# Optimization experiments

Hardware: AMD Instinct MI355X
Metric: run time of the kernel (lower is better)

## Reference

```python
import jax, jax.numpy as jnp
import numpy as np
import math

B, S, H, NH, NKV, HD = 1, 2048, 4096, 32, 8, 128
ROPE_THETA = 10000.0


def setup_inputs() -> dict:
    key = jax.random.key(0)
    ks = jax.random.split(key, 16)
    hidden_states = jax.random.normal(ks[0], (B, S, H), jnp.float32) * 0.02
    Wq = jax.random.normal(ks[1], (NH * HD, H), jnp.float32) * 0.02
    Wk = jax.random.normal(ks[2], (NKV * HD, H), jnp.float32) * 0.02
    Wv = jax.random.normal(ks[3], (NKV * HD, H), jnp.float32) * 0.02
    Wo = jax.random.normal(ks[4], (H, NH * HD), jnp.float32) * 0.02
    # RoPE cos/sin, HF Llama convention: emb = concat(freqs, freqs)
    inv_freq = 1.0 / (ROPE_THETA ** (jnp.arange(0, HD, 2, dtype=jnp.float32) / HD))
    pos = jnp.arange(S, dtype=jnp.float32)
    freqs = pos[:, None] * inv_freq[None, :]              # [S, HD/2]
    emb = jnp.concatenate([freqs, freqs], axis=-1)        # [S, HD]
    cos = jnp.cos(emb)[None]                              # [1, S, HD]
    sin = jnp.sin(emb)[None]
    # additive causal mask [B, 1, S, S]
    causal = jnp.tril(jnp.ones((S, S), dtype=bool))
    attention_mask = jnp.where(causal, 0.0, -1e9).astype(jnp.float32)[None, None]
    # reorder permutations (as written by GPTQ act-order reordering)
    perm = lambda k, n: jax.random.permutation(k, n).astype(jnp.int32)
    return {
        'hidden_states': hidden_states, 'Wq': Wq, 'Wk': Wk, 'Wv': Wv, 'Wo': Wo,
        'cos': cos, 'sin': sin, 'attention_mask': attention_mask,
        'q_order_col': perm(ks[5], H), 'q_order_row': perm(ks[6], NH * HD),
        'k_order_col': perm(ks[7], H), 'k_order_row': perm(ks[8], NKV * HD),
        'v_order_col': perm(ks[9], H), 'v_order_row': perm(ks[10], NKV * HD),
        'o_order_col': perm(ks[11], NH * HD), 'o_order_row': perm(ks[12], H),
    }


def _rotate_half(x):
    x1, x2 = jnp.split(x, 2, axis=-1)
    return jnp.concatenate([-x2, x1], axis=-1)


def reference(hidden_states, Wq, Wk, Wv, Wo, cos, sin, attention_mask,
              q_order_col, q_order_row, k_order_col, k_order_row,
              v_order_col, v_order_row, o_order_col, o_order_row):
    bsz, q_len, _ = hidden_states.shape
    # permuted projections: gather cols of input, GEMM, gather rows of output
    q = hidden_states[:, :, q_order_col] @ Wq.T
    q = q[:, :, q_order_row]
    k = hidden_states[:, :, k_order_col] @ Wk.T
    k = k[:, :, k_order_row]
    v = hidden_states[:, :, v_order_col] @ Wv.T
    v = v[:, :, v_order_row]
    q = q.reshape(bsz, q_len, NH, HD).transpose(0, 2, 1, 3)   # [B,NH,S,HD]
    k = k.reshape(bsz, q_len, NKV, HD).transpose(0, 2, 1, 3)  # [B,NKV,S,HD]
    v = v.reshape(bsz, q_len, NKV, HD).transpose(0, 2, 1, 3)
    # RoPE
    c = cos[:, None, :, :]  # [1,1,S,HD]
    s = sin[:, None, :, :]
    q = q * c + _rotate_half(q) * s
    k = k * c + _rotate_half(k) * s
    # repeat_kv for GQA
    rep = NH // NKV
    k = jnp.repeat(k, rep, axis=1)  # [B,NH,S,HD]
    v = jnp.repeat(v, rep, axis=1)
    # eager attention: full score matrix, fp32 softmax
    scores = jnp.einsum('bhqd,bhkd->bhqk', q, k) / math.sqrt(HD)
    scores = scores + attention_mask
    probs = jax.nn.softmax(scores.astype(jnp.float32), axis=-1).astype(q.dtype)
    # dropout p=0.0 (eval) -> identity
    attn = jnp.einsum('bhqk,bhkd->bhqd', probs, v)
    attn = attn.transpose(0, 2, 1, 3).reshape(bsz, q_len, NH * HD)
    out = attn[:, :, o_order_col] @ Wo.T
    out = out[:, :, o_order_row]
    return out
```

## Files before the change

kernel.cpp:

```cpp
#include <hip/hip_runtime.h>

typedef unsigned short u16;
typedef unsigned char u8;
typedef __bf16 bf16x8 __attribute__((ext_vector_type(8)));
typedef float f32x4 __attribute__((ext_vector_type(4)));
typedef int i32x4 __attribute__((ext_vector_type(4)));
typedef int i32x8 __attribute__((ext_vector_type(8)));

__device__ __forceinline__ u16 f2bf(float f) {
    unsigned u = __float_as_uint(f);
    unsigned r = (u + 0x7fffu + ((u >> 16) & 1u)) >> 16;
    return (u16)r;
}
__device__ __forceinline__ float bf2f(u16 h) {
    return __uint_as_float(((unsigned)h) << 16);
}
__device__ __forceinline__ unsigned pack_bf2(float lo, float hi) {
    unsigned a = __float_as_uint(hi) + 0x8000u;
    unsigned b = __float_as_uint(lo) + 0x8000u;
    return __builtin_amdgcn_perm(a, b, 0x07060302u);
}
__device__ __forceinline__ unsigned pack_fp8x4(float a, float b, float c, float d) {
    unsigned w = __builtin_amdgcn_cvt_pk_fp8_f32(a, b, 0, false);
    w = __builtin_amdgcn_cvt_pk_fp8_f32(c, d, w, true);
    return w;
}
__device__ __forceinline__ void async_copy16(const void* g, void* l) {
    __builtin_amdgcn_global_load_lds((__attribute__((address_space(1))) void*)(void*)g,
                                     (__attribute__((address_space(3))) void*)l, 16, 0, 0);
}

#define FP8_SCALE 64.0f
#define FP8_UNSCALE (1.0f / 4096.0f)


__global__ void inv4_k(const int* __restrict__ q, const int* __restrict__ k,
                       const int* __restrict__ v, const int* __restrict__ o,
                       int* __restrict__ invq, int* __restrict__ invk,
                       int* __restrict__ invv, int* __restrict__ invo) {
    int i = blockIdx.x * 256 + threadIdx.x;
    int a = i >> 12, j = i & 4095;
    const int* p = a == 0 ? q : a == 1 ? k : a == 2 ? v : o;
    int* inv = a == 0 ? invq : a == 1 ? invk : a == 2 ? invv : invo;
    inv[p[j]] = j;
}

__global__ __launch_bounds__(256) void permw4_k(
    const float* __restrict__ Wq, const float* __restrict__ Wk,
    const float* __restrict__ Wv, const float* __restrict__ Wo,
    const int* __restrict__ qor, const int* __restrict__ kor,
    const int* __restrict__ vor, const int* __restrict__ oor,
    const int* __restrict__ invq, const int* __restrict__ invk,
    const int* __restrict__ invv, const int* __restrict__ invo,
    u8* __restrict__ Wqkf8, u16* __restrict__ Wvp, u16* __restrict__ Wop) {
    __shared__ float rowbuf[4096];
    int j = blockIdx.x;
    const float* W; const int* rp; const int* inv; int row; int f8;
    u8* out8 = nullptr; u16* out16 = nullptr;
    if (j < 4096)      { W = Wq; rp = qor; inv = invq; row = j;        out8 = Wqkf8 + (size_t)j * 4096; f8 = 1; }
    else if (j < 5120) { W = Wk; rp = kor; inv = invk; row = j - 4096; out8 = Wqkf8 + (size_t)j * 4096; f8 = 1; }
    else if (j < 6144) { W = Wv; rp = vor; inv = invv; row = j - 5120; out16 = Wvp + (size_t)(j - 5120) * 4096; f8 = 0; }
    else               { W = Wo; rp = oor; inv = invo; row = j - 6144; out16 = Wop + (size_t)(j - 6144) * 4096; f8 = 0; }
    if (f8) {
        int hd = row & 127, b = hd >> 4;
        row = (row & ~127) | ((hd & 15) | ((b & 1) << 6) | ((b & 2) << 3) | ((hd & 64) >> 1));
    }
    const float4* wr4 = (const float4*)(W + (size_t)rp[row] * 4096);
#pragma unroll
    for (int t = 0; t < 4; t++)
        ((float4*)rowbuf)[threadIdx.x + t * 256] = wr4[threadIdx.x + t * 256];
    __syncthreads();
    if (f8) {
        int t = threadIdx.x;
        const int4* inv4p = (const int4*)inv;
        float v[16];
#pragma unroll
        for (int u = 0; u < 4; u++) {
            int4 ix = inv4p[t * 4 + u];
            v[4 * u + 0] = rowbuf[ix.x] * FP8_SCALE;
            v[4 * u + 1] = rowbuf[ix.y] * FP8_SCALE;
            v[4 * u + 2] = rowbuf[ix.z] * FP8_SCALE;
            v[4 * u + 3] = rowbuf[ix.w] * FP8_SCALE;
        }
        uint4 wv;
        wv.x = pack_fp8x4(v[0], v[1], v[2], v[3]);
        wv.y = pack_fp8x4(v[4], v[5], v[6], v[7]);
        wv.z = pack_fp8x4(v[8], v[9], v[10], v[11]);
        wv.w = pack_fp8x4(v[12], v[13], v[14], v[15]);
        int tb = (t & ~7) | ((t & 7) ^ (j & 7));
        ((uint4*)out8)[tb] = wv;
    } else {
        unsigned* o32 = (unsigned*)out16;
        const int2* inv2 = (const int2*)inv;
#pragma unroll
        for (int t = 0; t < 8; t++) {
            int c = threadIdx.x + t * 256;
            int2 ij = inv2[c];
            o32[c] = pack_bf2(rowbuf[ij.x], rowbuf[ij.y]);
        }
    }
}

__global__ __launch_bounds__(256) void cvt_k(const float* __restrict__ x,
                                             u16* __restrict__ Xb,
                                             u8* __restrict__ Xf8) {
    int row = blockIdx.x;
    int t = threadIdx.x;
    const float4* src = (const float4*)(x + (size_t)row * 4096);
    float v[16];
#pragma unroll
    for (int u = 0; u < 4; u++) {
        float4 a = src[t * 4 + u];
        v[4 * u + 0] = a.x; v[4 * u + 1] = a.y; v[4 * u + 2] = a.z; v[4 * u + 3] = a.w;
    }
    uint4 b0, b1;
    b0.x = pack_bf2(v[0], v[1]);  b0.y = pack_bf2(v[2], v[3]);
    b0.z = pack_bf2(v[4], v[5]);  b0.w = pack_bf2(v[6], v[7]);
    b1.x = pack_bf2(v[8], v[9]);  b1.y = pack_bf2(v[10], v[11]);
    b1.z = pack_bf2(v[12], v[13]); b1.w = pack_bf2(v[14], v[15]);
    uint4* ob = (uint4*)(Xb + (size_t)row * 4096);
    ob[t * 2] = b0;
    ob[t * 2 + 1] = b1;
    uint4 w8;
    w8.x = pack_fp8x4(v[0] * FP8_SCALE, v[1] * FP8_SCALE, v[2] * FP8_SCALE, v[3] * FP8_SCALE);
    w8.y = pack_fp8x4(v[4] * FP8_SCALE, v[5] * FP8_SCALE, v[6] * FP8_SCALE, v[7] * FP8_SCALE);
    w8.z = pack_fp8x4(v[8] * FP8_SCALE, v[9] * FP8_SCALE, v[10] * FP8_SCALE, v[11] * FP8_SCALE);
    w8.w = pack_fp8x4(v[12] * FP8_SCALE, v[13] * FP8_SCALE, v[14] * FP8_SCALE, v[15] * FP8_SCALE);
    int tb = (t & ~7) | ((t & 7) ^ (row & 7));
    ((uint4*)(Xf8 + (size_t)row * 4096))[tb] = w8;
}

__global__ __launch_bounds__(256) void vtr_k(const float* __restrict__ Vpart,
                                             u16* __restrict__ Vt) {
    __shared__ u16 t[64][65];
    int bx = blockIdx.x;
    int s0 = (bx & 31) * 64, c0 = (bx >> 5) * 64;
    int x = threadIdx.x & 63, y4 = threadIdx.x >> 6;
    const float* Vp0 = Vpart;
    const float* Vp1 = Vpart + (size_t)2048 * 1024;
    for (int i = 0; i < 16; i++) {
        int r = y4 * 16 + i;
        size_t idx = (size_t)(s0 + r) * 1024 + c0 + x;
        t[r][x] = f2bf(Vp0[idx] + Vp1[idx]);
    }
    __syncthreads();
    for (int i = 0; i < 16; i++) {
        int r = y4 * 16 + i;
        int xk = 4 * (x & 15) + (x >> 4);
        Vt[(size_t)(c0 + r) * 2048 + s0 + xk] = t[x][r];
    }
}


#define QKV_BAR() asm volatile("s_barrier" ::: "memory")

#define QK_STAGE(bufi, kt) do {                                                   \
    u8* la_ = S8 + (bufi) * 32768 + w * 4096;                                     \
    u8* lb_ = la_ + 16384;                                                        \
    const int k0_ = (kt) * 128;                                                   \
    _Pragma("unroll")                                                             \
    for (int t_ = 0; t_ < 4; t_++)                                                \
        async_copy16(AgQ + (size_t)t_ * 8 * 4096 + k0_, la_ + t_ * 1024);         \
    _Pragma("unroll")                                                             \
    for (int t_ = 0; t_ < 4; t_++)                                                \
        async_copy16(BgQ + (size_t)t_ * 8 * 4096 + k0_, lb_ + t_ * 1024);         \
} while (0)

#define QK_COMPUTE(bufi) do {                                                     \
    const u8* la_ = S8 + (bufi) * 32768;                                          \
    const u8* lb_ = la_ + 16384;                                                  \
    union { i32x8 v8; i32x4 v4[2]; } u_;                                          \
    i32x8 bfv[4], af0, af1;                                                       \
    _Pragma("unroll")                                                             \
    for (int j_ = 0; j_ < 4; j_++) {                                              \
        const int r_ = (wn + j_ * 16 + l16) * 128;                                \
        u_.v4[0] = *(const i32x4*)&lb_[r_ + s0b];                                 \
        u_.v4[1] = *(const i32x4*)&lb_[r_ + s1b];                                 \
        bfv[j_] = u_.v8;                                                          \
    }                                                                             \
    { const int r_ = (wm + l16) * 128;                                            \
      u_.v4[0] = *(const i32x4*)&la_[r_ + s0b];                                   \
      u_.v4[1] = *(const i32x4*)&la_[r_ + s1b]; af0 = u_.v8; }                    \
    { const int r_ = (wm + 16 + l16) * 128;                                       \
      u_.v4[0] = *(const i32x4*)&la_[r_ + s0b];                                   \
      u_.v4[1] = *(const i32x4*)&la_[r_ + s1b]; af1 = u_.v8; }                    \
    asm volatile("s_waitcnt lgkmcnt(0)" ::: "memory");                            \
    __builtin_amdgcn_sched_barrier(0);                                            \
    __builtin_amdgcn_s_setprio(1);                                                \
    _Pragma("unroll")                                                             \
    for (int j_ = 0; j_ < 4; j_++) {                                              \
        acc[0][j_] = __builtin_amdgcn_mfma_scale_f32_16x16x128_f8f6f4(af0, bfv[j_], acc[0][j_], 0, 0, 0, 0x7F7F7F7F, 0, 0x7F7F7F7F); \
        acc[1][j_] = __builtin_amdgcn_mfma_scale_f32_16x16x128_f8f6f4(af1, bfv[j_], acc[1][j_], 0, 0, 0, 0x7F7F7F7F, 0, 0x7F7F7F7F); \
    }                                                                             \
    __builtin_amdgcn_s_setprio(0);                                                \
    { const int r_ = (wm + 32 + l16) * 128;                                       \
      u_.v4[0] = *(const i32x4*)&la_[r_ + s0b];                                   \
      u_.v4[1] = *(const i32x4*)&la_[r_ + s1b]; af0 = u_.v8; }                    \
    { const int r_ = (wm + 48 + l16) * 128;                                       \
      u_.v4[0] = *(const i32x4*)&la_[r_ + s0b];                                   \
      u_.v4[1] = *(const i32x4*)&la_[r_ + s1b]; af1 = u_.v8; }                    \
    asm volatile("s_waitcnt lgkmcnt(0)" ::: "memory");                            \
    __builtin_amdgcn_sched_barrier(0);                                            \
    __builtin_amdgcn_s_setprio(1);                                                \
    _Pragma("unroll")                                                             \
    for (int j_ = 0; j_ < 4; j_++) {                                              \
        acc[2][j_] = __builtin_amdgcn_mfma_scale_f32_16x16x128_f8f6f4(af0, bfv[j_], acc[2][j_], 0, 0, 0, 0x7F7F7F7F, 0, 0x7F7F7F7F); \
        acc[3][j_] = __builtin_amdgcn_mfma_scale_f32_16x16x128_f8f6f4(af1, bfv[j_], acc[3][j_], 0, 0, 0, 0x7F7F7F7F, 0, 0x7F7F7F7F); \
    }                                                                             \
    __builtin_amdgcn_s_setprio(0);                                                \
} while (0)

#define V_STAGE(bufi, kt) do {                                                    \
    u16* a0_ = (u16*)(S8 + (bufi) * 32768);                                       \
    u16* a1_ = a0_ + 4096;                                                        \
    u16* b0_ = a0_ + 8192;                                                        \
    u16* b1_ = a0_ + 12288;                                                       \
    const int k0_ = (kt) * 64;                                                    \
    async_copy16(AgV + k0_,                          a0_ + w * 512);              \
    async_copy16(AgV + (size_t)64 * 4096 + k0_,      a0_ + (w + 4) * 512);        \
    async_copy16(AgV + k0_ + 32,                     a1_ + w * 512);              \
    async_copy16(AgV + (size_t)64 * 4096 + k0_ + 32, a1_ + (w + 4) * 512);        \
    async_copy16(BgV + k0_,                          b0_ + w * 512);              \
    async_copy16(BgV + (size_t)64 * 4096 + k0_,      b0_ + (w + 4) * 512);        \
    async_copy16(BgV + k0_ + 32,                     b1_ + w * 512);              \
    async_copy16(BgV + (size_t)64 * 4096 + k0_ + 32, b1_ + (w + 4) * 512);        \
} while (0)

#define V_COMPUTE(bufi) do {                                                      \
    const u16* base_ = (const u16*)(S8 + (bufi) * 32768);                         \
    _Pragma("unroll")                                                             \
    for (int kk_ = 0; kk_ < 2; kk_++) {                                           \
        const u16* la_ = base_ + kk_ * 4096;                                      \
        const u16* lb_ = base_ + 8192 + kk_ * 4096;                               \
        bf16x8 af[4], bfv[4];                                                     \
        _Pragma("unroll")                                                         \
        for (int i_ = 0; i_ < 4; i_++)                                            \
            af[i_] = *(const bf16x8*)&la_[(wm + i_ * 16 + l16) * 32 + quad * 8];  \
        _Pragma("unroll")                                                         \
        for (int j_ = 0; j_ < 4; j_++)                                            \
            bfv[j_] = *(const bf16x8*)&lb_[(wn + j_ * 16 + l16) * 32 + quad * 8]; \
        asm volatile("s_waitcnt lgkmcnt(0)" ::: "memory");                        \
        __builtin_amdgcn_sched_barrier(0);                                        \
        __builtin_amdgcn_s_setprio(1);                                            \
        _Pragma("unroll")                                                         \
        for (int i_ = 0; i_ < 4; i_++)                                            \
            _Pragma("unroll")                                                     \
            for (int j_ = 0; j_ < 4; j_++)                                        \
                acc[i_][j_] = __builtin_amdgcn_mfma_f32_16x16x32_bf16(af[i_], bfv[j_], acc[i_][j_], 0, 0, 0); \
        __builtin_amdgcn_s_setprio(0);                                            \
    }                                                                             \
} while (0)

__global__ __launch_bounds__(256, 2) void gemm_qkv_k(const u8* __restrict__ Xf8,
                                                     const u16* __restrict__ Xb,
                                                     const u8* __restrict__ Wqk,
                                                     const u16* __restrict__ Wv,
                                                     u16* __restrict__ QKV,
                                                     float* __restrict__ Vpart,
                                                     const float* __restrict__ cosv,
                                                     const float* __restrict__ sinv) {
    extern __shared__ u8 S8[];
    const int tid = threadIdx.x;
    const int w = tid >> 6, lane = tid & 63;
    const int quad = lane >> 4, l16 = lane & 15;
    const int bm0 = blockIdx.y * 128;
    const int wm = (w >> 1) * 64, wn = (w & 1) * 64;
    const int swz = l16 & 7;
    const int s0b = ((quad * 2) ^ swz) * 16;
    const int s1b = ((quad * 2 + 1) ^ swz) * 16;

    if (blockIdx.x < 40) {
        const int bn0 = blockIdx.x * 128;
        const u8* AgQ = Xf8 + (size_t)(bm0 + w * 32 + (lane >> 3)) * 4096 + (lane & 7) * 16;
        const u8* BgQ = Wqk + (size_t)(bn0 + w * 32 + (lane >> 3)) * 4096 + (lane & 7) * 16;
        f32x4 acc[4][4] = {};

        QK_STAGE(0, 0);
        QK_STAGE(1, 1);
        asm volatile("s_waitcnt vmcnt(8)" ::: "memory");
        QKV_BAR();
        int cur = 0;
        for (int t = 0; t < 30; ++t) {
            QK_COMPUTE(cur);
            QKV_BAR();
            QK_STAGE(cur, t + 2);
            asm volatile("s_waitcnt vmcnt(8)" ::: "memory");
            QKV_BAR();
            cur ^= 1;
        }
        QK_COMPUTE(0);
        asm volatile("s_waitcnt vmcnt(0)" ::: "memory");
        QKV_BAR();
        QK_COMPUTE(1);

        const float qsc = (bn0 < 4096) ? 0.08838834764831845f : 1.0f;
        const int hb = (wn ? 32 : 0) + l16;
#pragma unroll
        for (int i = 0; i < 4; i++) {
            const int row = bm0 + wm + i * 16 + quad * 4;
#pragma unroll
            for (int jp = 0; jp < 2; jp++) {
                const int d1 = hb + jp * 16;
                const int ce = bn0 + wn + jp * 32 + l16;
#pragma unroll
                for (int r = 0; r < 4; r++) {
                    const int s = row + r;
                    const float c  = cosv[s * 128 + d1];
                    const float sn = sinv[s * 128 + d1];
                    const float x1 = acc[i][jp * 2][r]     * FP8_UNSCALE;
                    const float x2 = acc[i][jp * 2 + 1][r] * FP8_UNSCALE;
                    QKV[(size_t)s * 6144 + ce]      = f2bf((x1 * c - x2 * sn) * qsc);
                    QKV[(size_t)s * 6144 + ce + 16] = f2bf((x2 * c + x1 * sn) * qsc);
                }
            }
        }
    } else {
        const int vx = blockIdx.x - 40;
        const int bn0 = (vx & 7) * 128;
        const int kslice = vx >> 3;
        const int kb = kslice * 2048;
        const int r0 = w * 16 + (lane >> 2);
        const int c0 = (lane & 3) * 8;
        const u16* AgV = Xb + (size_t)(bm0 + r0) * 4096 + kb + c0;
        const u16* BgV = Wv + (size_t)(bn0 + r0) * 4096 + kb + c0;
        f32x4 acc[4][4] = {};

        V_STAGE(0, 0);
        V_STAGE(1, 1);
        asm volatile("s_waitcnt vmcnt(8)" ::: "memory");
        QKV_BAR();
        int cur = 0;
        for (int t = 0; t < 30; ++t) {
            V_COMPUTE(cur);
            QKV_BAR();
            V_STAGE(cur, t + 2);
            asm volatile("s_waitcnt vmcnt(8)" ::: "memory");
            QKV_BAR();
            cur ^= 1;
        }
        V_COMPUTE(0);
        asm volatile("s_waitcnt vmcnt(0)" ::: "memory");
        QKV_BAR();
        V_COMPUTE(1);

        float* Vp = Vpart + (size_t)kslice * 2048 * 1024;
#pragma unroll
        for (int i = 0; i < 4; i++) {
            const int row = bm0 + wm + i * 16 + quad * 4;
#pragma unroll
            for (int j = 0; j < 4; j++) {
                const int col = bn0 + wn + j * 16 + l16;
#pragma unroll
                for (int r = 0; r < 4; r++)
                    Vp[(size_t)(row + r) * 1024 + col] = acc[i][j][r];
            }
        }
    }
}


#define GO_STAGE(bufi, kt) do {                                                   \
    u16* la_ = S + (bufi) * 24576;                                                \
    u16* lb_ = la_ + 16384;                                                       \
    const int k0_ = (kt) * 64;                                                    \
    _Pragma("unroll")                                                             \
    for (int u = 0; u < 4; u++)                                                   \
        async_copy16(Asrc + (size_t)u * 64 * 4096 + k0_, la_ + u * 4096 + sdst);  \
    _Pragma("unroll")                                                             \
    for (int u = 0; u < 2; u++)                                                   \
        async_copy16(Bsrc + (size_t)u * 64 * 4096 + k0_, lb_ + u * 4096 + sdst);  \
} while (0)

#define GO_COMPUTE(bufi) do {                                                     \
    const u16* la_ = S + (bufi) * 24576;                                          \
    const u16* lb_ = la_ + 16384;                                                 \
    bf16x8 bfr[4][2], afr[2][2];                                                  \
    _Pragma("unroll")                                                             \
    for (int j = 0; j < 4; j++) {                                                 \
        const int rb_ = (wn + j * 16 + l16) * 64;                                 \
        bfr[j][0] = *(const bf16x8*)&lb_[rb_ + o0];                               \
        bfr[j][1] = *(const bf16x8*)&lb_[rb_ + o1];                               \
    }                                                                             \
    _Pragma("unroll")                                                             \
    for (int i = 0; i < 2; i++) {                                                 \
        const int ra_ = (wm + i * 16 + l16) * 64;                                 \
        afr[i][0] = *(const bf16x8*)&la_[ra_ + o0];                               \
        afr[i][1] = *(const bf16x8*)&la_[ra_ + o1];                               \
    }                                                                             \
    asm volatile("s_waitcnt lgkmcnt(0)" ::: "memory");                            \
    __builtin_amdgcn_sched_barrier(0);                                            \
    __builtin_amdgcn_s_setprio(1);                                                \
    _Pragma("unroll")                                                             \
    for (int i = 0; i < 2; i++)                                                   \
        _Pragma("unroll")                                                         \
        for (int j = 0; j < 4; j++) {                                             \
            acc[i][j] = __builtin_amdgcn_mfma_f32_16x16x32_bf16(afr[i][0], bfr[j][0], acc[i][j], 0, 0, 0); \
            acc[i][j] = __builtin_amdgcn_mfma_f32_16x16x32_bf16(afr[i][1], bfr[j][1], acc[i][j], 0, 0, 0); \
        }                                                                         \
    __builtin_amdgcn_s_setprio(0);                                                \
    _Pragma("unroll")                                                             \
    for (int i = 0; i < 2; i++) {                                                 \
        const int ra_ = (wm + (i + 2) * 16 + l16) * 64;                           \
        afr[i][0] = *(const bf16x8*)&la_[ra_ + o0];                               \
        afr[i][1] = *(const bf16x8*)&la_[ra_ + o1];                               \
    }                                                                             \
    asm volatile("s_waitcnt lgkmcnt(0)" ::: "memory");                            \
    __builtin_amdgcn_sched_barrier(0);                                            \
    __builtin_amdgcn_s_setprio(1);                                                \
    _Pragma("unroll")                                                             \
    for (int i = 0; i < 2; i++)                                                   \
        _Pragma("unroll")                                                         \
        for (int j = 0; j < 4; j++) {                                             \
            acc[i + 2][j] = __builtin_amdgcn_mfma_f32_16x16x32_bf16(afr[i][0], bfr[j][0], acc[i + 2][j], 0, 0, 0); \
            acc[i + 2][j] = __builtin_amdgcn_mfma_f32_16x16x32_bf16(afr[i][1], bfr[j][1], acc[i + 2][j], 0, 0, 0); \
        }                                                                         \
    __builtin_amdgcn_s_setprio(0);                                                \
} while (0)

#define GO_BAR() asm volatile("s_barrier" ::: "memory")

__global__ __launch_bounds__(512, 2) void gemm_o_k(const u16* __restrict__ A,
                                                   const u16* __restrict__ B,
                                                   float* __restrict__ Out) {
    extern __shared__ u16 S[];
    const int tid = threadIdx.x;
    const int w = tid >> 6, lane = tid & 63;
    const int quad = lane >> 4, l16 = lane & 15;
    const int linear = blockIdx.y * 32 + blockIdx.x;
    const int wgid = (linear & 7) * 32 + (linear >> 3);
    const int bm0 = (wgid >> 5) * 256;
    const int bn0 = (wgid & 31) * 128;
    const int wm = (w >> 1) * 64;
    const int wn = (w & 1) * 64;
    const int sr = tid >> 3;
    const int scg = ((tid & 7) ^ (sr & 7)) * 8;
    const int sdst = tid * 8;
    const u16* Asrc = A + (size_t)(bm0 + sr) * 4096 + scg;
    const u16* Bsrc = B + (size_t)(bn0 + sr) * 4096 + scg;
    const int swz = l16 & 7;
    const int o0 = (quad ^ swz) * 8;
    const int o1 = ((4 | quad) ^ swz) * 8;

    f32x4 acc[4][4] = {};

    GO_STAGE(0, 0);
    GO_STAGE(1, 1);
    GO_STAGE(2, 2);
    asm volatile("s_waitcnt vmcnt(12)" ::: "memory");
    GO_BAR();

    int cur = 0;
    for (int t = 0; t < 61; ++t) {
        GO_COMPUTE(cur);
        GO_BAR();
        GO_STAGE(cur, t + 3);
        asm volatile("s_waitcnt vmcnt(12)" ::: "memory");
        GO_BAR();
        cur = (cur == 2) ? 0 : cur + 1;
    }
    GO_COMPUTE(1);
    asm volatile("s_waitcnt vmcnt(6)" ::: "memory");
    GO_BAR();
    GO_COMPUTE(2);
    asm volatile("s_waitcnt vmcnt(0)" ::: "memory");
    GO_BAR();
    GO_COMPUTE(0);

#pragma unroll
    for (int i = 0; i < 4; i++) {
        const int row = bm0 + wm + i * 16 + quad * 4;
#pragma unroll
        for (int j = 0; j < 4; j++) {
            const int col = bn0 + wn + j * 16 + l16;
#pragma unroll
            for (int r = 0; r < 4; r++)
                Out[(size_t)(row + r) * 4096 + col] = acc[i][j][r];
        }
    }
}


__global__ __launch_bounds__(256) void attn_k(const u16* __restrict__ Qb,
                                              const u16* __restrict__ Kb,
                                              const u16* __restrict__ Vt,
                                              u16* __restrict__ Ob,
                                              int qstride, int kstride) {
    __shared__ u16 ldsK[4 * 64 * 32];
    __shared__ u16 ldsV[2 * 128 * 32];
    __shared__ u16 ldsP[4][32 * 72];
    const int h = blockIdx.x;
    const int qt = (int)gridDim.y - 1 - (int)blockIdx.y;
    const int kvh = h >> 2;
    const int tid = threadIdx.x;
    const int w = tid >> 6, lane = tid & 63;
    const int quad = lane >> 4, l16 = lane & 15;
    const int q0 = qt * 128;
    const int wrow = q0 + w * 32;

    bf16x8 qf[2][4];
#pragma unroll
    for (int mi = 0; mi < 2; mi++)
#pragma unroll
        for (int kk = 0; kk < 4; kk++)
            qf[mi][kk] = *(const bf16x8*)&Qb[(size_t)(wrow + mi * 16 + l16) * qstride +
                                             h * 128 + kk * 32 + quad * 8];

    const u16* kp[4]; const u16* vp[4];
    u16* ldk[4]; u16* ldv[4];
#pragma unroll
    for (int t = 0; t < 4; t++) {
        int wl = w + t * 4;
        int kk = wl >> 2, part = wl & 3;
        kp[t] = Kb + (size_t)(part * 16 + (lane >> 2)) * kstride + kvh * 128 + kk * 32 + (lane & 3) * 8;
        int ks2 = wl >> 3, p2 = wl & 7;
        vp[t] = Vt + (size_t)(kvh * 128 + p2 * 16 + (lane >> 2)) * 2048 + ks2 * 32 + (lane & 3) * 8;
        ldk[t] = ldsK + wl * 512;
        ldv[t] = ldsV + wl * 512;
    }

    f32x4 acc_o[2][8] = {};
    float lrow[2][4] = {};

    const int nk = 2 * (qt + 1);
    for (int kn = 0; kn < nk; kn++) {
        const int g0 = kn * 64;
#pragma unroll
        for (int t = 0; t < 4; t++) async_copy16(kp[t], ldk[t]);
#pragma unroll
        for (int t = 0; t < 4; t++) async_copy16(vp[t], ldv[t]);
#pragma unroll
        for (int t = 0; t < 4; t++) { kp[t] += (size_t)64 * kstride; vp[t] += 64; }
        __syncthreads();

        if (g0 <= wrow + 31) {
            f32x4 accs[2][4] = {};
#pragma unroll
            for (int kk = 0; kk < 4; kk++) {
                bf16x8 bfrag[4];
#pragma unroll
                for (int ni = 0; ni < 4; ni++)
                    bfrag[ni] = *(const bf16x8*)&ldsK[kk * 2048 + (ni * 16 + l16) * 32 + quad * 8];
                __builtin_amdgcn_s_setprio(1);
#pragma unroll
                for (int mi = 0; mi < 2; mi++)
#pragma unroll
                    for (int ni = 0; ni < 4; ni++)
                        accs[mi][ni] = __builtin_amdgcn_mfma_f32_16x16x32_bf16(
                            qf[mi][kk], bfrag[ni], accs[mi][ni], 0, 0, 0);
                __builtin_amdgcn_s_setprio(0);
            }
            const bool diag = (g0 + 63 > wrow);
            int kidx[4];
#pragma unroll
            for (int ni = 0; ni < 4; ni++) kidx[ni] = g0 + ni * 16 + l16;
#pragma unroll
            for (int mi = 0; mi < 2; mi++) {
#pragma unroll
                for (int r = 0; r < 4; r++) {
                    const int qrow = wrow + mi * 16 + quad * 4 + r;
                    float p[4];
#pragma unroll
                    for (int ni = 0; ni < 4; ni++) {
                        float s = accs[mi][ni][r];
                        if (diag && (kidx[ni] > qrow)) s = -1e30f;
                        p[ni] = __expf(s);
                    }
                    lrow[mi][r] += (p[0] + p[1]) + (p[2] + p[3]);
                    uint2 pk;
                    pk.x = pack_bf2(p[0], p[1]);
                    pk.y = pack_bf2(p[2], p[3]);
                    *(uint2*)&ldsP[w][(mi * 16 + quad * 4 + r) * 72 + l16 * 4] = pk;
                }
            }
#pragma unroll
            for (int ks = 0; ks < 2; ks++) {
                bf16x8 pa[2];
#pragma unroll
                for (int mi = 0; mi < 2; mi++)
                    pa[mi] = *(const bf16x8*)&ldsP[w][(mi * 16 + l16) * 72 + ks * 32 + quad * 8];
                __builtin_amdgcn_s_setprio(1);
#pragma unroll
                for (int oj = 0; oj < 8; oj++) {
                    bf16x8 vb = *(const bf16x8*)&ldsV[ks * 4096 + (oj * 16 + l16) * 32 + quad * 8];
#pragma unroll
                    for (int mi = 0; mi < 2; mi++)
                        acc_o[mi][oj] = __builtin_amdgcn_mfma_f32_16x16x32_bf16(
                            pa[mi], vb, acc_o[mi][oj], 0, 0, 0);
                }
                __builtin_amdgcn_s_setprio(0);
            }
        }
        __syncthreads();
    }
#pragma unroll
    for (int mi = 0; mi < 2; mi++)
#pragma unroll
        for (int r = 0; r < 4; r++) {
            float l = lrow[mi][r];
            l += __shfl_xor(l, 1);
            l += __shfl_xor(l, 2);
            l += __shfl_xor(l, 4);
            l += __shfl_xor(l, 8);
            const float inv = 1.0f / l;
            const int qrow = wrow + mi * 16 + quad * 4 + r;
#pragma unroll
            for (int oj = 0; oj < 8; oj++)
                Ob[(size_t)qrow * 4096 + h * 128 + oj * 16 + l16] =
                    f2bf(acc_o[mi][oj][r] * inv);
        }
}


extern "C" void kernel_launch(void* const* d_in, const int* in_sizes, int n_in,
                              void* d_out, int out_size, void* d_ws, size_t ws_size,
                              hipStream_t stream) {
    (void)in_sizes; (void)n_in; (void)out_size; (void)ws_size;
    const float* hidden = (const float*)d_in[0];
    const float* Wq = (const float*)d_in[1];
    const float* Wk = (const float*)d_in[2];
    const float* Wv = (const float*)d_in[3];
    const float* Wo = (const float*)d_in[4];
    const float* cosv = (const float*)d_in[5];
    const float* sinv = (const float*)d_in[6];
    const int* qoc = (const int*)d_in[8];
    const int* qor = (const int*)d_in[9];
    const int* koc = (const int*)d_in[10];
    const int* kor = (const int*)d_in[11];
    const int* voc = (const int*)d_in[12];
    const int* vor = (const int*)d_in[13];
    const int* ooc = (const int*)d_in[14];
    const int* oor = (const int*)d_in[15];

    char* ws = (char*)d_ws;
    size_t off = 0;
    int* invq = (int*)(ws + off); off += 16384;
    int* invk = (int*)(ws + off); off += 16384;
    int* invv = (int*)(ws + off); off += 16384;
    int* invo = (int*)(ws + off); off += 16384;
    u16* Wop   = (u16*)(ws + off); off += (size_t)4096 * 4096 * 2;
    u16* Xb    = (u16*)(ws + off); off += (size_t)2048 * 4096 * 2;
    u8*  Wqkf8 = (u8*)(ws + off);  off += (size_t)5120 * 4096;
    u16* Wvp   = (u16*)(ws + off); off += (size_t)1024 * 4096 * 2;
    u8*  Xf8   = (u8*)(ws + off);  off += (size_t)2048 * 4096;
    u16* QKVb  = (u16*)(ws + off); off += (size_t)2048 * 6144 * 2;
    u16* Vtb   = (u16*)(ws + off); off += (size_t)1024 * 2048 * 2;
    float* Vpart = (float*)(ws + off); off += (size_t)2 * 2048 * 1024 * 4;
    u16* Attb  = Xb;

    inv4_k<<<64, 256, 0, stream>>>(qoc, koc, voc, ooc, invq, invk, invv, invo);
    permw4_k<<<10240, 256, 0, stream>>>(Wq, Wk, Wv, Wo, qor, kor, vor, oor,
                                        invq, invk, invv, invo, Wqkf8, Wvp, Wop);
    cvt_k<<<2048, 256, 0, stream>>>(hidden, Xb, Xf8);

    gemm_qkv_k<<<dim3(56, 16), 256, 65536, stream>>>(Xf8, Xb, Wqkf8, Wvp, QKVb, Vpart,
                                                     cosv, sinv);

    vtr_k<<<512, 256, 0, stream>>>(Vpart, Vtb);

    attn_k<<<dim3(32, 16), 256, 0, stream>>>(QKVb, QKVb + 4096, Vtb, Attb, 6144, 6144);

    gemm_o_k<<<dim3(32, 8), 512, 147456, stream>>>(Attb, Wop, (float*)d_out);
}
```

Before: 471.7 us.

## Pair causal query tiles per block with 8 waves and exp2 softmax

The attention kernel now uses 512 threads (8 waves of 16 query rows each) and each block handles two query tiles, the tile at index 15-y and the tile at index y. This balances causal work across a grid of 256 blocks. The Q scale constant now folds in log2(e) so the softmax can use the hardware exp2 instead of __expf. Each wave now has half as many MFMA rows per K/V tile load, which lowers per-wave reuse of the K/V fragments, and each block processes its two tiles one after the other with the same barriers.

New measurement: 468.0 us. No clear change (-0.8%).

```diff
diff --git a/kernel.cpp b/kernel.cpp
--- a/kernel.cpp
+++ b/kernel.cpp
@@ -293,7 +293,7 @@
         QKV_BAR();
         QK_COMPUTE(1);
 
-        const float qsc = (bn0 < 4096) ? 0.08838834764831845f : 1.0f;
+        const float qsc = (bn0 < 4096) ? 0.1275174f : 1.0f;
         const int hb = (wn ? 32 : 0) + l16;
 #pragma unroll
         for (int i = 0; i < 4; i++) {
@@ -480,134 +480,129 @@
 }
 
 
-__global__ __launch_bounds__(256) void attn_k(const u16* __restrict__ Qb,
+__global__ __launch_bounds__(512) void attn_k(const u16* __restrict__ Qb,
                                               const u16* __restrict__ Kb,
                                               const u16* __restrict__ Vt,
                                               u16* __restrict__ Ob,
                                               int qstride, int kstride) {
     __shared__ u16 ldsK[4 * 64 * 32];
     __shared__ u16 ldsV[2 * 128 * 32];
-    __shared__ u16 ldsP[4][32 * 72];
+    __shared__ u16 ldsP[8][16 * 72];
     const int h = blockIdx.x;
-    const int qt = (int)gridDim.y - 1 - (int)blockIdx.y;
     const int kvh = h >> 2;
     const int tid = threadIdx.x;
     const int w = tid >> 6, lane = tid & 63;
     const int quad = lane >> 4, l16 = lane & 15;
-    const int q0 = qt * 128;
-    const int wrow = q0 + w * 32;
-
-    bf16x8 qf[2][4];
-#pragma unroll
-    for (int mi = 0; mi < 2; mi++)
-#pragma unroll
-        for (int kk = 0; kk < 4; kk++)
-            qf[mi][kk] = *(const bf16x8*)&Qb[(size_t)(wrow + mi * 16 + l16) * qstride +
-                                             h * 128 + kk * 32 + quad * 8];
-
-    const u16* kp[4]; const u16* vp[4];
-    u16* ldk[4]; u16* ldv[4];
-#pragma unroll
-    for (int t = 0; t < 4; t++) {
-        int wl = w + t * 4;
+
+    const u16* kp0[2]; const u16* vp0[2];
+    u16* ldk[2]; u16* ldv[2];
+#pragma unroll
+    for (int t = 0; t < 2; t++) {
+        int wl = w + t * 8;
         int kk = wl >> 2, part = wl & 3;
-        kp[t] = Kb + (size_t)(part * 16 + (lane >> 2)) * kstride + kvh * 128 + kk * 32 + (lane & 3) * 8;
+        kp0[t] = Kb + (size_t)(part * 16 + (lane >> 2)) * kstride + kvh * 128 + kk * 32 + (lane & 3) * 8;
         int ks2 = wl >> 3, p2 = wl & 7;
-        vp[t] = Vt + (size_t)(kvh * 128 + p2 * 16 + (lane >> 2)) * 2048 + ks2 * 32 + (lane & 3) * 8;
+        vp0[t] = Vt + (size_t)(kvh * 128 + p2 * 16 + (lane >> 2)) * 2048 + ks2 * 32 + (lane & 3) * 8;
         ldk[t] = ldsK + wl * 512;
         ldv[t] = ldsV + wl * 512;
     }
 
-    f32x4 acc_o[2][8] = {};
-    float lrow[2][4] = {};
-
-    const int nk = 2 * (qt + 1);
-    for (int kn = 0; kn < nk; kn++) {
-        const int g0 = kn * 64;
-#pragma unroll
-        for (int t = 0; t < 4; t++) async_copy16(kp[t], ldk[t]);
-#pragma unroll
-        for (int t = 0; t < 4; t++) async_copy16(vp[t], ldv[t]);
-#pragma unroll
-        for (int t = 0; t < 4; t++) { kp[t] += (size_t)64 * kstride; vp[t] += 64; }
-        __syncthreads();
-
-        if (g0 <= wrow + 31) {
-            f32x4 accs[2][4] = {};
-#pragma unroll
-            for (int kk = 0; kk < 4; kk++) {
-                bf16x8 bfrag[4];
-#pragma unroll
-                for (int ni = 0; ni < 4; ni++)
-                    bfrag[ni] = *(const bf16x8*)&ldsK[kk * 2048 + (ni * 16 + l16) * 32 + quad * 8];
-                __builtin_amdgcn_s_setprio(1);
-#pragma unroll
-                for (int mi = 0; mi < 2; mi++)
+#pragma unroll
+    for (int ph = 0; ph < 2; ph++) {
+        const int qt = ph == 0 ? (15 - (int)blockIdx.y) : (int)blockIdx.y;
+        const int q0 = qt * 128;
+        const int wrow = q0 + w * 16;
+
+        bf16x8 qf[4];
+#pragma unroll
+        for (int kk = 0; kk < 4; kk++)
+            qf[kk] = *(const bf16x8*)&Qb[(size_t)(wrow + l16) * qstride +
+                                         h * 128 + kk * 32 + quad * 8];
+
+        const u16* kp[2]; const u16* vp[2];
+        kp[0] = kp0[0]; kp[1] = kp0[1];
+        vp[0] = vp0[0]; vp[1] = vp0[1];
+
+        f32x4 acc_o[8] = {};
+        float lrow[4] = {};
+
+        const int nk = 2 * (qt + 1);
+        for (int kn = 0; kn < nk; kn++) {
+            const int g0 = kn * 64;
+            async_copy16(kp[0], ldk[0]);
+            async_copy16(kp[1], ldk[1]);
+            async_copy16(vp[0], ldv[0]);
+            async_copy16(vp[1], ldv[1]);
+            kp[0] += (size_t)64 * kstride; kp[1] += (size_t)64 * kstride;
+            vp[0] += 64; vp[1] += 64;
+            __syncthreads();
+
+            if (g0 <= wrow + 15) {
+                f32x4 accs[4] = {};
+#pragma unroll
+                for (int kk = 0; kk < 4; kk++) {
+                    bf16x8 bfrag[4];
 #pragma unroll
                     for (int ni = 0; ni < 4; ni++)
-                        accs[mi][ni] = __builtin_amdgcn_mfma_f32_16x16x32_bf16(
-                            qf[mi][kk], bfrag[ni], accs[mi][ni], 0, 0, 0);
-                __builtin_amdgcn_s_setprio(0);
-            }
-            const bool diag = (g0 + 63 > wrow);
-            int kidx[4];
-#pragma unroll
-            for (int ni = 0; ni < 4; ni++) kidx[ni] = g0 + ni * 16 + l16;
-#pragma unroll
-            for (int mi = 0; mi < 2; mi++) {
+                        bfrag[ni] = *(const bf16x8*)&ldsK[kk * 2048 + (ni * 16 + l16) * 32 + quad * 8];
+                    __builtin_amdgcn_s_setprio(1);
+#pragma unroll
+                    for (int ni = 0; ni < 4; ni++)
+                        accs[ni] = __builtin_amdgcn_mfma_f32_16x16x32_bf16(
+                            qf[kk], bfrag[ni], accs[ni], 0, 0, 0);
+                    __builtin_amdgcn_s_setprio(0);
+                }
+                const bool diag = (g0 + 63 > wrow);
+                int kidx[4];
+#pragma unroll
+                for (int ni = 0; ni < 4; ni++) kidx[ni] = g0 + ni * 16 + l16;
 #pragma unroll
                 for (int r = 0; r < 4; r++) {
-                    const int qrow = wrow + mi * 16 + quad * 4 + r;
+                    const int qrow = wrow + quad * 4 + r;
                     float p[4];
 #pragma unroll
                     for (int ni = 0; ni < 4; ni++) {
-                        float s = accs[mi][ni][r];
+                        float s = accs[ni][r];
                         if (diag && (kidx[ni] > qrow)) s = -1e30f;
-                        p[ni] = __expf(s);
+                        p[ni] = __builtin_amdgcn_exp2f(s);
                     }
-                    lrow[mi][r] += (p[0] + p[1]) + (p[2] + p[3]);
+                    lrow[r] += (p[0] + p[1]) + (p[2] + p[3]);
                     uint2 pk;
                     pk.x = pack_bf2(p[0], p[1]);
                     pk.y = pack_bf2(p[2], p[3]);
-                    *(uint2*)&ldsP[w][(mi * 16 + quad * 4 + r) * 72 + l16 * 4] = pk;
+                    *(uint2*)&ldsP[w][(quad * 4 + r) * 72 + l16 * 4] = pk;
+                }
+#pragma unroll
+                for (int ks = 0; ks < 2; ks++) {
+                    bf16x8 pa = *(const bf16x8*)&ldsP[w][l16 * 72 + ks * 32 + quad * 8];
+                    __builtin_amdgcn_s_setprio(1);
+#pragma unroll
+                    for (int oj = 0; oj < 8; oj++) {
+                        bf16x8 vb = *(const bf16x8*)&ldsV[ks * 4096 + (oj * 16 + l16) * 32 + quad * 8];
+                        acc_o[oj] = __builtin_amdgcn_mfma_f32_16x16x32_bf16(
+                            pa, vb, acc_o[oj], 0, 0, 0);
+                    }
+                    __builtin_amdgcn_s_setprio(0);
                 }
             }
-#pragma unroll
-            for (int ks = 0; ks < 2; ks++) {
-                bf16x8 pa[2];
-#pragma unroll
-                for (int mi = 0; mi < 2; mi++)
-                    pa[mi] = *(const bf16x8*)&ldsP[w][(mi * 16 + l16) * 72 + ks * 32 + quad * 8];
-                __builtin_amdgcn_s_setprio(1);
-#pragma unroll
-                for (int oj = 0; oj < 8; oj++) {
-                    bf16x8 vb = *(const bf16x8*)&ldsV[ks * 4096 + (oj * 16 + l16) * 32 + quad * 8];
-#pragma unroll
-                    for (int mi = 0; mi < 2; mi++)
-                        acc_o[mi][oj] = __builtin_amdgcn_mfma_f32_16x16x32_bf16(
-                            pa[mi], vb, acc_o[mi][oj], 0, 0, 0);
-                }
-                __builtin_amdgcn_s_setprio(0);
-            }
-        }
-        __syncthreads();
-    }
-#pragma unroll
-    for (int mi = 0; mi < 2; mi++)
+            __syncthreads();
+        }
+
 #pragma unroll
         for (int r = 0; r < 4; r++) {
-            float l = lrow[mi][r];
+            float l = lrow[r];
             l += __shfl_xor(l, 1);
             l += __shfl_xor(l, 2);
             l += __shfl_xor(l, 4);
             l += __shfl_xor(l, 8);
             const float inv = 1.0f / l;
-            const int qrow = wrow + mi * 16 + quad * 4 + r;
+            const int qrow = wrow + quad * 4 + r;
 #pragma unroll
             for (int oj = 0; oj < 8; oj++)
                 Ob[(size_t)qrow * 4096 + h * 128 + oj * 16 + l16] =
-                    f2bf(acc_o[mi][oj][r] * inv);
-        }
+                    f2bf(acc_o[oj][r] * inv);
+        }
+    }
 }
 
 
@@ -657,7 +652,7 @@
 
     vtr_k<<<512, 256, 0, stream>>>(Vpart, Vtb);
 
-    attn_k<<<dim3(32, 16), 256, 0, stream>>>(QKVb, QKVb + 4096, Vtb, Attb, 6144, 6144);
+    attn_k<<<dim3(32, 8), 512, 0, stream>>>(QKVb, QKVb + 4096, Vtb, Attb, 6144, 6144);
 
     gemm_o_k<<<dim3(32, 8), 512, 147456, stream>>>(Attb, Wop, (float*)d_out);
 }
```
